# Kernel optimization log

Measured on AMD Instinct MI355X. Metric: run time of the kernel, lower is better.

## Reference

```python
import jax, jax.numpy as jnp
import numpy as np

BN_EPS = 1e-5

def _ste_sign(x):
    # forward: sign in {-1,+1}; backward: clipped straight-through (grad 1 on [-1,1])
    s = jnp.where(x >= 0, 1.0, -1.0).astype(x.dtype)
    c = jnp.clip(x, -1.0, 1.0)
    return c + jax.lax.stop_gradient(s - c)

def setup_inputs() -> dict:
    key = jax.random.key(0)
    ks = jax.random.split(key, 8)
    N, C, H, W = 32, 256, 56, 56
    x = jax.random.normal(ks[0], (N, C, H, W), dtype=jnp.float32)
    bias0 = jax.random.normal(ks[1], (C,), dtype=jnp.float32) * 0.1
    w = jax.random.normal(ks[2], (C, C, 1, 1), dtype=jnp.float32) * 0.05
    gamma = jnp.ones((C,), dtype=jnp.float32)
    beta = jnp.zeros((C,), dtype=jnp.float32)
    bias1 = jax.random.normal(ks[3], (C,), dtype=jnp.float32) * 0.1
    alpha = jnp.full((C,), 0.25, dtype=jnp.float32)  # PReLU init
    bias2 = jax.random.normal(ks[4], (C,), dtype=jnp.float32) * 0.1
    return {"x": x, "bias0": bias0, "w": w, "gamma": gamma, "beta": beta,
            "bias1": bias1, "alpha": alpha, "bias2": bias2}

def reference(x, bias0, w, gamma, beta, bias1, alpha, bias2):
    ch = lambda v: v[None, :, None, None]
    # move0: learnable per-channel bias
    out = x + ch(bias0)
    # binary activation: sign (STE)
    out = _ste_sign(out)
    # binarized 1x1 conv: w_bin = mean(|w|) per out-channel * sign(w)
    scale = jnp.mean(jnp.abs(w), axis=(1, 2, 3))              # [O]
    wb = scale[:, None] * _ste_sign(w[:, :, 0, 0])            # [O, C]
    out = jnp.einsum('nchw,oc->nohw', out, wb)                # 1x1 conv
    # bn1: batch statistics (training-mode math)
    mu = jnp.mean(out, axis=(0, 2, 3), keepdims=True)
    var = jnp.var(out, axis=(0, 2, 3), keepdims=True)
    out = ch(gamma) * (out - mu) * jax.lax.rsqrt(var + BN_EPS) + ch(beta)
    # residual add (downsample is None)
    out = out + x
    # move1 -> PReLU -> move2
    out = out + ch(bias1)
    out = jnp.where(out > 0, out, ch(alpha) * out)
    out = out + ch(bias2)
    return out
```

## Files before the change

### kernel.cpp

```cpp
#include <hip/hip_runtime.h>
#include <stdint.h>

typedef unsigned long long u64;
typedef unsigned int u32;

constexpr int kC  = 256;
constexpr int kHW = 3136;
constexpr int kN  = 32;
constexpr int kP  = kN * kHW;
constexpr int kPosPk = 64;
constexpr int kBlkPk = kP / kPosPk;
constexpr int kPosSt = 128;
constexpr int kBlkSt = kP / kPosSt;
constexpr int kRedBlk = 16;
constexpr int kRedRows = 49;

constexpr size_t OFF_T     = 0;
constexpr size_t OFF_SCALE = 8192;
constexpr size_t OFF_SUMD  = 9216;
constexpr size_t OFF_SUMD2 = 11264;
constexpr size_t OFF_S     = 13312;
constexpr size_t OFF_PS    = 3224576;
constexpr size_t OFF_PQ    = 4027392;

struct alignas(16) U64x2 { u64 x, y; };

__global__ __launch_bounds__(256) void prep_kernel(
    const float* __restrict__ w, char* __restrict__ ws) {
  int t = threadIdx.x;
  int b = blockIdx.x;
  u64*   T     = (u64*)(ws + OFF_T);
  float* scale = (float*)(ws + OFF_SCALE);
  int kk = t >> 6, ln = t & 63;
  if (b == 0) {
    ((u64*)(ws + OFF_SUMD))[t]  = 0ull;
    ((u64*)(ws + OFF_SUMD2))[t] = 0ull;
  }
  __shared__ float part[4][16];
#pragma unroll
  for (int i = 0; i < 16; ++i) {
    int o = b * 16 + i;
    float v = w[o * kC + kk * 64 + ln];
    u64 m = __ballot(v >= 0.0f);
    float a = fabsf(v);
#pragma unroll
    for (int s = 32; s > 0; s >>= 1) a += __shfl_xor(a, s, 64);
    if (ln == 0) { T[kk * 256 + o] = m; part[kk][i] = a; }
  }
  __syncthreads();
  if (t < 16) {
    int o = b * 16 + t;
    scale[o] = (part[0][t] + part[1][t] + part[2][t] + part[3][t]) * (1.0f / 256.0f);
  }
}

__global__ __launch_bounds__(256) void pack_kernel(
    const float* __restrict__ x, const float* __restrict__ bias0,
    char* __restrict__ ws) {
  int t = threadIdx.x;
  int b = blockIdx.x;
  int k    = __builtin_amdgcn_readfirstlane(t >> 6);
  int lane = t & 63;
  u32 p  = (u32)b * (u32)kPosPk + (u32)lane;
  u32 n  = p / kHW;
  u32 hw = p - n * kHW;
  const float* xp = x + (size_t)n * kC * kHW + (size_t)(k * 64) * kHW + hw;
  const float* bp = bias0 + k * 64;

  u64 m = 0;
#pragma unroll 32
  for (int i = 0; i < 64; ++i) {
    float v = __builtin_nontemporal_load(xp + (size_t)i * kHW) + bp[i];
    m |= (u64)(v >= 0.0f) << i;
  }
  u64* S = (u64*)(ws + OFF_S);
  S[(size_t)k * kP + p] = m;
}

__global__ __launch_bounds__(256) void stats_kernel(char* __restrict__ ws) {
  int o = threadIdx.x;
  const u64* T = (const u64*)(ws + OFF_T);
  u64 t0 = T[o], t1 = T[256 + o], t2 = T[512 + o], t3 = T[768 + o];
  const u64* S = (const u64*)(ws + OFF_S);
  u32 pb = blockIdx.x * (u32)kPosSt;

  int summ = 0, summ2 = 0;
#pragma unroll 8
  for (int j = 0; j < kPosSt; j += 2) {
    u32 p = pb + j;
    U64x2 a0 = *(const U64x2*)&S[p];
    U64x2 a1 = *(const U64x2*)&S[kP + p];
    U64x2 a2 = *(const U64x2*)&S[2 * kP + p];
    U64x2 a3 = *(const U64x2*)&S[3 * kP + p];
    int ka = __popcll(a0.x ^ t0) + __popcll(a1.x ^ t1) +
             __popcll(a2.x ^ t2) + __popcll(a3.x ^ t3);
    int kb = __popcll(a0.y ^ t0) + __popcll(a1.y ^ t1) +
             __popcll(a2.y ^ t2) + __popcll(a3.y ^ t3);
    int ma = 128 - ka, mb = 128 - kb;
    summ  += ma + mb;
    summ2 += ma * ma + mb * mb;
  }
  ((int*)(ws + OFF_PS))[blockIdx.x * 256 + o] = summ;
  ((int*)(ws + OFF_PQ))[blockIdx.x * 256 + o] = summ2;
}

__global__ __launch_bounds__(256) void reduce_kernel(char* __restrict__ ws) {
  int t = threadIdx.x;
  int b = blockIdx.x;
  const int* PS = (const int*)(ws + OFF_PS);
  const int* PQ = (const int*)(ws + OFF_PQ);
  long long s = 0, q = 0;
#pragma unroll 7
  for (int r = 0; r < kRedRows; ++r) {
    int row = b * kRedRows + r;
    s += PS[row * 256 + t];
    q += PQ[row * 256 + t];
  }
  atomicAdd((u64*)(ws + OFF_SUMD) + t,  (u64)(long long)(2 * s));
  atomicAdd((u64*)(ws + OFF_SUMD2) + t, (u64)(long long)(4 * q));
}

__global__ __launch_bounds__(256) void finalize_kernel(
    const float* __restrict__ x, const float* __restrict__ gamma,
    const float* __restrict__ beta, const float* __restrict__ bias1,
    const float* __restrict__ alpha, const float* __restrict__ bias2,
    const char* __restrict__ ws, float* __restrict__ out) {
  __shared__ u64    ldsT[256][4];
  __shared__ float4 ldsC[256];

  int t = threadIdx.x;
  {
    const u64* T = (const u64*)(ws + OFF_T);
#pragma unroll
    for (int q = 0; q < 4; ++q) ldsT[t][q] = T[q * 256 + t];

    const float*     scale = (const float*)(ws + OFF_SCALE);
    const long long* sumd  = (const long long*)(ws + OFF_SUMD);
    const long long* sumd2 = (const long long*)(ws + OFF_SUMD2);
    double inv  = 1.0 / (double)kP;
    double md   = (double)sumd[t] * inv;
    double e2   = (double)sumd2[t] * inv;
    double vard = e2 - md * md;
    float sc  = scale[t];
    float mu  = sc * (float)md;
    float var = sc * sc * (float)vard;
    float rs  = rsqrtf(var + 1e-5f);
    float g   = gamma[t];
    float cA  = g * rs * sc;
    float cB  = beta[t] - g * rs * mu + bias1[t];
    ldsC[t] = make_float4(2.0f * cA, cB, alpha[t], bias2[t]);
  }
  __syncthreads();

  int k    = __builtin_amdgcn_readfirstlane(t >> 6);
  int lane = t & 63;
  u32 p  = blockIdx.x * (u32)kPosPk + (u32)lane;
  u32 n  = p / kHW;
  u32 hw = p - n * kHW;

  const u64* S = (const u64*)(ws + OFF_S);
  u64 s0 = S[p];
  u64 s1 = S[kP + p];
  u64 s2 = S[2 * kP + p];
  u64 s3 = S[3 * kP + p];

  const float* xp = x   + (size_t)n * kC * kHW + (size_t)(k * 64) * kHW + hw;
  float*       op = out + (size_t)n * kC * kHW + (size_t)(k * 64) * kHW + hw;

#pragma unroll 8
  for (int i = 0; i < 64; ++i) {
    int o = k * 64 + i;
    u64 w0 = ldsT[o][0], w1 = ldsT[o][1], w2 = ldsT[o][2], w3 = ldsT[o][3];
    int kx = __popcll(s0 ^ w0) + __popcll(s1 ^ w1) +
             __popcll(s2 ^ w2) + __popcll(s3 ^ w3);
    float4 cc = ldsC[o];
    float xv = __builtin_nontemporal_load(xp + (size_t)i * kHW);
    float u  = fmaf(cc.x, (float)(128 - kx), cc.y) + xv;
    float r  = u > 0.0f ? u : cc.z * u;
    __builtin_nontemporal_store(r + cc.w, op + (size_t)i * kHW);
  }
}

extern "C" void kernel_launch(void* const* d_in, const int* in_sizes, int n_in,
                              void* d_out, int out_size, void* d_ws, size_t ws_size,
                              hipStream_t stream) {
  const float* x     = (const float*)d_in[0];
  const float* bias0 = (const float*)d_in[1];
  const float* w     = (const float*)d_in[2];
  const float* gamma = (const float*)d_in[3];
  const float* beta  = (const float*)d_in[4];
  const float* bias1 = (const float*)d_in[5];
  const float* alpha = (const float*)d_in[6];
  const float* bias2 = (const float*)d_in[7];
  float* out = (float*)d_out;
  char*  ws  = (char*)d_ws;

  hipLaunchKernelGGL(prep_kernel, dim3(16), dim3(256), 0, stream, w, ws);
  hipLaunchKernelGGL(pack_kernel, dim3(kBlkPk), dim3(256), 0, stream,
                     x, bias0, ws);
  hipLaunchKernelGGL(stats_kernel, dim3(kBlkSt), dim3(256), 0, stream, ws);
  hipLaunchKernelGGL(reduce_kernel, dim3(kRedBlk), dim3(256), 0, stream, ws);
  hipLaunchKernelGGL(finalize_kernel, dim3(kBlkPk), dim3(256), 0, stream,
                     x, gamma, beta, bias1, alpha, bias2, ws, out);
}
```

Measured before the change: 246.3 us.

## Fuse sign-packing and BN statistics into one kernel; drop nontemporal x loads

```diff
diff --git a/kernel.cpp b/kernel.cpp
--- a/kernel.cpp
+++ b/kernel.cpp
@@ -8,12 +8,10 @@
 constexpr int kHW = 3136;
 constexpr int kN  = 32;
 constexpr int kP  = kN * kHW;
-constexpr int kPosPk = 64;
-constexpr int kBlkPk = kP / kPosPk;
-constexpr int kPosSt = 128;
-constexpr int kBlkSt = kP / kPosSt;
-constexpr int kRedBlk = 16;
-constexpr int kRedRows = 49;
+constexpr int kPos = 64;
+constexpr int kBlk = kP / kPos;
+constexpr int kRedBlk  = 16;
+constexpr int kRedRows = kBlk / kRedBlk;
 
 constexpr size_t OFF_T     = 0;
 constexpr size_t OFF_SCALE = 8192;
@@ -21,7 +19,7 @@
 constexpr size_t OFF_SUMD2 = 11264;
 constexpr size_t OFF_S     = 13312;
 constexpr size_t OFF_PS    = 3224576;
-constexpr size_t OFF_PQ    = 4027392;
+constexpr size_t OFF_PQ    = 4830208;
 
 struct alignas(16) U64x2 { u64 x, y; };
 
@@ -54,14 +52,15 @@
   }
 }
 
-__global__ __launch_bounds__(256) void pack_kernel(
+__global__ __launch_bounds__(256) void pack_stats_kernel(
     const float* __restrict__ x, const float* __restrict__ bias0,
     char* __restrict__ ws) {
   int t = threadIdx.x;
   int b = blockIdx.x;
   int k    = __builtin_amdgcn_readfirstlane(t >> 6);
   int lane = t & 63;
-  u32 p  = (u32)b * (u32)kPosPk + (u32)lane;
+  u32 pb = (u32)b * (u32)kPos;
+  u32 p  = pb + (u32)lane;
   u32 n  = p / kHW;
   u32 hw = p - n * kHW;
   const float* xp = x + (size_t)n * kC * kHW + (size_t)(k * 64) * kHW + hw;
@@ -70,28 +69,24 @@
   u64 m = 0;
 #pragma unroll 32
   for (int i = 0; i < 64; ++i) {
-    float v = __builtin_nontemporal_load(xp + (size_t)i * kHW) + bp[i];
+    float v = xp[(size_t)i * kHW] + bp[i];
     m |= (u64)(v >= 0.0f) << i;
   }
   u64* S = (u64*)(ws + OFF_S);
   S[(size_t)k * kP + p] = m;
-}
 
-__global__ __launch_bounds__(256) void stats_kernel(char* __restrict__ ws) {
-  int o = threadIdx.x;
+  __syncthreads();
+
   const u64* T = (const u64*)(ws + OFF_T);
-  u64 t0 = T[o], t1 = T[256 + o], t2 = T[512 + o], t3 = T[768 + o];
-  const u64* S = (const u64*)(ws + OFF_S);
-  u32 pb = blockIdx.x * (u32)kPosSt;
-
+  u64 t0 = T[t], t1 = T[256 + t], t2 = T[512 + t], t3 = T[768 + t];
   int summ = 0, summ2 = 0;
 #pragma unroll 8
-  for (int j = 0; j < kPosSt; j += 2) {
-    u32 p = pb + j;
-    U64x2 a0 = *(const U64x2*)&S[p];
-    U64x2 a1 = *(const U64x2*)&S[kP + p];
-    U64x2 a2 = *(const U64x2*)&S[2 * kP + p];
-    U64x2 a3 = *(const U64x2*)&S[3 * kP + p];
+  for (int j = 0; j < kPos; j += 2) {
+    u32 q = pb + j;
+    U64x2 a0 = *(const U64x2*)&S[q];
+    U64x2 a1 = *(const U64x2*)&S[kP + q];
+    U64x2 a2 = *(const U64x2*)&S[2 * kP + q];
+    U64x2 a3 = *(const U64x2*)&S[3 * kP + q];
     int ka = __popcll(a0.x ^ t0) + __popcll(a1.x ^ t1) +
              __popcll(a2.x ^ t2) + __popcll(a3.x ^ t3);
     int kb = __popcll(a0.y ^ t0) + __popcll(a1.y ^ t1) +
@@ -100,8 +95,8 @@
     summ  += ma + mb;
     summ2 += ma * ma + mb * mb;
   }
-  ((int*)(ws + OFF_PS))[blockIdx.x * 256 + o] = summ;
-  ((int*)(ws + OFF_PQ))[blockIdx.x * 256 + o] = summ2;
+  ((int*)(ws + OFF_PS))[b * 256 + t] = summ;
+  ((int*)(ws + OFF_PQ))[b * 256 + t] = summ2;
 }
 
 __global__ __launch_bounds__(256) void reduce_kernel(char* __restrict__ ws) {
@@ -154,7 +149,7 @@
 
   int k    = __builtin_amdgcn_readfirstlane(t >> 6);
   int lane = t & 63;
-  u32 p  = blockIdx.x * (u32)kPosPk + (u32)lane;
+  u32 p  = blockIdx.x * (u32)kPos + (u32)lane;
   u32 n  = p / kHW;
   u32 hw = p - n * kHW;
 
@@ -174,7 +169,7 @@
     int kx = __popcll(s0 ^ w0) + __popcll(s1 ^ w1) +
              __popcll(s2 ^ w2) + __popcll(s3 ^ w3);
     float4 cc = ldsC[o];
-    float xv = __builtin_nontemporal_load(xp + (size_t)i * kHW);
+    float xv = xp[(size_t)i * kHW];
     float u  = fmaf(cc.x, (float)(128 - kx), cc.y) + xv;
     float r  = u > 0.0f ? u : cc.z * u;
     __builtin_nontemporal_store(r + cc.w, op + (size_t)i * kHW);
@@ -196,10 +191,9 @@
   char*  ws  = (char*)d_ws;
 
   hipLaunchKernelGGL(prep_kernel, dim3(16), dim3(256), 0, stream, w, ws);
-  hipLaunchKernelGGL(pack_kernel, dim3(kBlkPk), dim3(256), 0, stream,
+  hipLaunchKernelGGL(pack_stats_kernel, dim3(kBlk), dim3(256), 0, stream,
                      x, bias0, ws);
-  hipLaunchKernelGGL(stats_kernel, dim3(kBlkSt), dim3(256), 0, stream, ws);
   hipLaunchKernelGGL(reduce_kernel, dim3(kRedBlk), dim3(256), 0, stream, ws);
-  hipLaunchKernelGGL(finalize_kernel, dim3(kBlkPk), dim3(256), 0, stream,
+  hipLaunchKernelGGL(finalize_kernel, dim3(kBlk), dim3(256), 0, stream,
                      x, gamma, beta, bias1, alpha, bias2, ws, out);
 }
```

Result: slower. 255.6 us (+3.8%).
